# Optimization experiments

Hardware: AMD Instinct MI355X
Metric: run time of the kernel (lower is better)

Reference implementation:

```python
import jax, jax.numpy as jnp
import numpy as np

# ---- static config (matches init_kwargs) ----
OC, IC, K, S, PAD = 128, 64, 3, 1, 1
M, T, R = 5, 8, 2.5            # ALSH m, table_size, LSH bucket width r
SPAN = K * K * IC              # kernel_span = 576


def setup_inputs() -> dict:
    key = jax.random.key(0)
    k1, k2, k3, k4 = jax.random.split(key, 4)
    # xavier_uniform on the (OC, SPAN) kernel matrix
    bound = float(np.sqrt(6.0 / (OC + SPAN)))
    kernels = jax.random.uniform(k1, (OC, SPAN), minval=-bound, maxval=bound, dtype=jnp.float32)
    a = jax.random.normal(k2, (SPAN + M,), dtype=jnp.float32)          # LSH projection
    b = jax.random.uniform(k3, (), minval=0.0, maxval=R, dtype=jnp.float32)  # LSH offset
    x = jax.random.normal(k4, (16, IC, 56, 56), dtype=jnp.float32)
    return {"x": x, "kernels": kernels, "a": a, "b": b, "mode": 0}


def _im2col(x):
    # [B, SPAN, H2, W2] with feature order (C, kh, kw)
    p = jax.lax.conv_general_dilated_patches(x, (K, K), (S, S), [(PAD, PAD), (PAD, PAD)])
    B, _, H2, W2 = p.shape
    # patch matrix [SPAN, B*H2*W2]
    return p.transpose(1, 0, 2, 3).reshape(SPAN, -1), B, H2, W2


def _bucket(h):
    # floor((h+b)/r); fmod table_size; abs  (matches torch .fmod_ then .abs_)
    return jnp.abs(jnp.fmod(h.astype(jnp.int32), T))


def reference(x, kernels, a, b, mode):
    patch_matr, B, H2, W2 = _im2col(x)            # [SPAN, N], N = B*H2*W2

    # ---- vote: hash every patch column with Q-augmentation (append m halves) ----
    v = a[:SPAN] @ patch_matr + 0.5 * jnp.sum(a[SPAN:])      # [N]
    votes = _bucket(jnp.floor((v + b) / R))
    counts = jnp.zeros((T,), jnp.int32).at[votes].add(1)
    bucket = jnp.argmax(counts)                               # most common bucket

    # ---- hash table: hash each kernel row with P-augmentation (norm powers) ----
    norms2 = jnp.sum(kernels * kernels, axis=1)               # ||k||^2, [OC]
    powers = jnp.stack([norms2 ** (2 ** i) for i in range(M)], axis=1)  # ||k||^{2,4,...,2^M}
    hk = kernels @ a[:SPAN] + powers @ a[SPAN:]               # [OC]
    kidx = _bucket(jnp.floor((hk + b) / R))                   # bucket of each kernel

    # ---- select kernels in the winning bucket; scale by |rows|/OC ----
    mask = (kidx == bucket).astype(x.dtype)                   # [OC]
    cnt = jnp.sum(mask)
    # original gathers the selected rows (variable oc); we scatter back to the
    # full OC channels (zeros for inactive kernels) for static shapes.
    # empty bucket -> dense conv with all kernels, no rescale.
    factor = jnp.where(cnt > 0, mask * (OC / jnp.maximum(cnt, 1.0)), jnp.ones_like(mask))

    out = (kernels * factor[:, None]) @ patch_matr            # [OC, N]
    out = out.reshape(OC, B, H2 * W2).transpose(1, 0, 2)
    return out.reshape(B, OC, H2, W2)
```

## Files before the change

### kernel.cpp

```cpp
#include <hip/hip_runtime.h>
#include <math.h>

#define IC 64
#define OC 128
#define HH 56
#define WW 56
#define BATCH 16
#define HP 58
#define HW (HH*WW)
#define NPIX (BATCH*HW)
#define SPAN 576
#define TSIZE 8
#define VBLOCKS 196

typedef unsigned short ushort_t;
typedef unsigned int uint_t;
typedef __attribute__((ext_vector_type(8))) __bf16 bf16x8;
typedef __attribute__((ext_vector_type(4))) float f32x4;

__device__ __forceinline__ ushort_t bf16_rne(float f) {
  uint_t u = __builtin_bit_cast(uint_t, f);
  u += 0x7FFFu + ((u >> 16) & 1u);
  return (ushort_t)(u >> 16);
}

__global__ void pad_kernel(const float* __restrict__ x, ushort_t* __restrict__ xpad) {
  int idx = blockIdx.x * 256 + threadIdx.x;
  if (idx >= BATCH * HP * HP) return;
  int b = idx / (HP * HP);
  int rem = idx % (HP * HP);
  int y = rem / HP, xw = rem % HP;
  int h = y - 1, w = xw - 1;
  bool inb = ((unsigned)h < (unsigned)HH) && ((unsigned)w < (unsigned)WW);
  const float* src = x + (size_t)b * IC * HW + (inb ? h * WW + w : 0);
  uint_t* dst = (uint_t*)(xpad + (size_t)idx * IC);
  #pragma unroll
  for (int c2 = 0; c2 < IC / 2; ++c2) {
    float f0 = inb ? src[(2 * c2) * HW] : 0.0f;
    float f1 = inb ? src[(2 * c2 + 1) * HW] : 0.0f;
    dst[c2] = (uint_t)bf16_rne(f0) | ((uint_t)bf16_rne(f1) << 16);
  }
}

__global__ __launch_bounds__(256)
void tstage_kernel(const float* __restrict__ x, const float* __restrict__ a,
                   float* __restrict__ tbuf) {
  int n = blockIdx.x * 256 + threadIdx.x;
  int b = n / HW, p = n % HW;
  const float* xb = x + (size_t)b * IC * HW + p;
  float t9[9] = {0, 0, 0, 0, 0, 0, 0, 0, 0};
  #pragma unroll
  for (int c = 0; c < IC; ++c) {
    float xv = xb[(size_t)c * HW];
    #pragma unroll
    for (int tap = 0; tap < 9; ++tap) t9[tap] += a[c * 9 + tap] * xv;
  }
  float* tb = tbuf + (size_t)b * 9 * HW + p;
  #pragma unroll
  for (int tap = 0; tap < 9; ++tap) tb[(size_t)tap * HW] = t9[tap];
}

__global__ void vote2_kernel(const float* __restrict__ tbuf, const float* __restrict__ a,
                             const float* __restrict__ bptr, int* __restrict__ hist_partial) {
  __shared__ int hist[TSIZE];
  const int t = threadIdx.x;
  if (t < TSIZE) hist[t] = 0;
  __syncthreads();
  int n = blockIdx.x * 256 + t;
  int b = n / HW, p = n % HW;
  int h = p / WW, w = p % WW;
  const float* tb = tbuf + ((size_t)b * 9) * HW;
  float v = 0.0f;
  #pragma unroll
  for (int kh = 0; kh < 3; ++kh) {
    int yy = h + kh - 1;
    if ((unsigned)yy < (unsigned)HH) {
      #pragma unroll
      for (int kw = 0; kw < 3; ++kw) {
        int xx = w + kw - 1;
        if ((unsigned)xx < (unsigned)WW) v += tb[(size_t)(kh * 3 + kw) * HW + yy * WW + xx];
      }
    }
  }
  float tail = 0.5f * (a[576] + a[577] + a[578] + a[579] + a[580]);
  int hi = (int)floorf((v + tail + bptr[0]) / 2.5f);
  int r = hi % TSIZE;
  if (r < 0) r = -r;
  atomicAdd(&hist[r], 1);
  __syncthreads();
  if (t < TSIZE) hist_partial[blockIdx.x * TSIZE + t] = hist[t];
}

__global__ void w2row_kernel(const float* __restrict__ kernels, const float* __restrict__ a,
                             const float* __restrict__ bptr, ushort_t* __restrict__ w2,
                             int* __restrict__ rbucket) {
  const int r = blockIdx.x, t = threadIdx.x;
  const float* row = kernels + (size_t)r * SPAN;
  float d = 0.0f, n2 = 0.0f;
  #pragma unroll
  for (int k0 = 0; k0 < 3; ++k0) {
    int k = k0 * 256 + t;
    if (k < SPAN) { float kv = row[k]; d += kv * a[k]; n2 += kv * kv; }
  }
  __shared__ float red0[256], red1[256];
  red0[t] = d; red1[t] = n2;
  __syncthreads();
  for (int s = 128; s > 0; s >>= 1) {
    if (t < s) { red0[t] += red0[t + s]; red1[t] += red1[t + s]; }
    __syncthreads();
  }
  if (t == 0) {
    float hk = red0[0], p = red1[0];
    #pragma unroll
    for (int i = 0; i < 5; ++i) { hk += p * a[SPAN + i]; p = p * p; }
    int hi = (int)floorf((hk + bptr[0]) / 2.5f);
    int rr = hi % TSIZE;
    if (rr < 0) rr = -rr;
    rbucket[r] = rr;
  }
  #pragma unroll
  for (int j0 = 0; j0 < 3; ++j0) {
    int j = j0 * 256 + t;
    if (j < SPAN) {
      int tap = j >> 6, c = j & 63;
      w2[(size_t)r * SPAN + j] = bf16_rne(row[c * 9 + tap]);
    }
  }
}

__global__ __launch_bounds__(256, 4)
void gemm_kernel(const ushort_t* __restrict__ w2, const ushort_t* __restrict__ xpad,
                 const int* __restrict__ hist_partial, const int* __restrict__ rbucket,
                 float* __restrict__ out) {
  __shared__ ushort_t As[128 * 64];
  __shared__ ushort_t Bs[64 * 64];
  __shared__ float factor_s[OC];
  __shared__ int counts_s[TSIZE];
  __shared__ int cnt_w[4];
  const int tid = threadIdx.x;
  const int wave = tid >> 6, lane = tid & 63;
  const int n0 = blockIdx.x * 64;
  const int wm = wave * 32;

  const int srow = lane >> 3;
  const int sch = (lane & 7) ^ srow;

  int agbase[4], bgbase[2];
  #pragma unroll
  for (int i = 0; i < 4; ++i) {
    int row = wm + i * 8 + srow;
    agbase[i] = row * SPAN + sch * 8;
  }
  #pragma unroll
  for (int i = 0; i < 2; ++i) {
    int brow = wave * 16 + i * 8 + srow;
    int n = n0 + brow;
    int b = n / HW;
    int rem = n % HW;
    int h = rem / WW, w = rem % WW;
    bgbase[i] = ((b * HP + h) * HP + w) * IC + sch * 8;
  }

  f32x4 acc[2][4] = {};

  for (int tap = 0; tap < 9; ++tap) {
    const int kh = tap / 3, kw = tap % 3;
    const int toffA = tap * 64;
    const int toffB = (kh * HP + kw) * IC;
    __syncthreads();
    #pragma unroll
    for (int i = 0; i < 4; ++i)
      __builtin_amdgcn_global_load_lds(
          (const __attribute__((address_space(1))) void*)(w2 + agbase[i] + toffA),
          (__attribute__((address_space(3))) void*)(As + (wm + i * 8) * 64), 16, 0, 0);
    #pragma unroll
    for (int i = 0; i < 2; ++i)
      __builtin_amdgcn_global_load_lds(
          (const __attribute__((address_space(1))) void*)(xpad + bgbase[i] + toffB),
          (__attribute__((address_space(3))) void*)(Bs + (wave * 16 + i * 8) * 64), 16, 0, 0);
    __syncthreads();
    #pragma unroll
    for (int kk = 0; kk < 2; ++kk) {
      const int jf = kk * 4 + (lane >> 4);
      bf16x8 af[2], bfr[4];
      #pragma unroll
      for (int m = 0; m < 2; ++m) {
        int row = wm + m * 16 + (lane & 15);
        int slot = row * 8 + (jf ^ (row & 7));
        af[m] = *(const bf16x8*)(As + slot * 8);
      }
      #pragma unroll
      for (int n = 0; n < 4; ++n) {
        int col = n * 16 + (lane & 15);
        int slot = col * 8 + (jf ^ (col & 7));
        bfr[n] = *(const bf16x8*)(Bs + slot * 8);
      }
      #pragma unroll
      for (int m = 0; m < 2; ++m)
        #pragma unroll
        for (int n = 0; n < 4; ++n)
          acc[m][n] = __builtin_amdgcn_mfma_f32_16x16x32_bf16(af[m], bfr[n], acc[m][n], 0, 0, 0);
    }
  }

  if (tid < TSIZE) counts_s[tid] = 0;
  __syncthreads();
  {
    int bin = tid >> 5;
    int s = 0;
    for (int k = (tid & 31); k < VBLOCKS; k += 32) s += hist_partial[k * TSIZE + bin];
    atomicAdd(&counts_s[bin], s);
  }
  __syncthreads();
  int best = counts_s[0], bi = 0;
  #pragma unroll
  for (int i = 1; i < TSIZE; ++i) { int c = counts_s[i]; if (c > best) { best = c; bi = i; } }
  int isin = (tid < OC) ? ((rbucket[tid] == bi) ? 1 : 0) : 0;
  unsigned long long bal = __ballot(isin != 0);
  if (lane == 0) cnt_w[wave] = __popcll(bal);
  __syncthreads();
  int cnt = cnt_w[0] + cnt_w[1] + cnt_w[2] + cnt_w[3];
  if (tid < OC)
    factor_s[tid] = (cnt > 0) ? (isin ? 128.0f / (float)cnt : 0.0f) : 1.0f;
  __syncthreads();

  #pragma unroll
  for (int n = 0; n < 4; ++n) {
    int np = n0 + n * 16 + (lane & 15);
    int b = np / HW;
    int rem = np % HW;
    float* obase = out + ((size_t)b * OC) * HW + rem;
    #pragma unroll
    for (int m = 0; m < 2; ++m) {
      int ocb = wm + m * 16 + (lane >> 4) * 4;
      #pragma unroll
      for (int r = 0; r < 4; ++r) {
        obase[(size_t)(ocb + r) * HW] = acc[m][n][r] * factor_s[ocb + r];
      }
    }
  }
}

extern "C" void kernel_launch(void* const* d_in, const int* in_sizes, int n_in,
                              void* d_out, int out_size, void* d_ws, size_t ws_size,
                              hipStream_t stream) {
  (void)in_sizes; (void)n_in; (void)out_size; (void)ws_size;
  const float* x = (const float*)d_in[0];
  const float* kernels = (const float*)d_in[1];
  const float* a = (const float*)d_in[2];
  const float* b = (const float*)d_in[3];
  float* out = (float*)d_out;

  char* ws = (char*)d_ws;
  int* rbucket = (int*)ws;
  int* hist_partial = (int*)(ws + 512);
  ushort_t* w2 = (ushort_t*)(ws + 8192);
  float* tbuf = (float*)(ws + 8192 + 147456);
  ushort_t* xpad = (ushort_t*)(ws + 8192 + 147456 + 1806336);

  pad_kernel<<<211, 256, 0, stream>>>(x, xpad);
  tstage_kernel<<<VBLOCKS, 256, 0, stream>>>(x, a, tbuf);
  vote2_kernel<<<VBLOCKS, 256, 0, stream>>>(tbuf, a, b, hist_partial);
  w2row_kernel<<<OC, 256, 0, stream>>>(kernels, a, b, w2, rbucket);
  gemm_kernel<<<NPIX / 64, 256, 0, stream>>>(w2, xpad, hist_partial, rbucket, out);
}
```

Baseline: 121.9 us.

## Fuse pad, vote and weight-prep kernels into one block-dispatched prep kernel

Merges the padding, tap-projection, vote-histogram and weight-row kernels into a single launch. Blocks pick their role by block index. The vote path now keeps the per-tap projections of a two-row band plus halo rows in shared memory instead of writing and re-reading a global tbuf. This removes three launches and a global round trip. In exchange, each band recomputes the projections of its halo rows, roughly doubling that arithmetic, and the number of histogram partials the GEMM epilogue must sum grows to 448.

```diff
diff --git a/kernel.cpp b/kernel.cpp
--- a/kernel.cpp
+++ b/kernel.cpp
@@ -11,7 +11,10 @@
 #define NPIX (BATCH*HW)
 #define SPAN 576
 #define TSIZE 8
-#define VBLOCKS 196
+#define PADBLK 211
+#define VBANDS 28
+#define VBLOCKS (BATCH*VBANDS)
+#define NBLK1 (PADBLK + VBLOCKS + OC)
 
 typedef unsigned short ushort_t;
 typedef unsigned int uint_t;
@@ -24,106 +27,107 @@
   return (ushort_t)(u >> 16);
 }
 
-__global__ void pad_kernel(const float* __restrict__ x, ushort_t* __restrict__ xpad) {
-  int idx = blockIdx.x * 256 + threadIdx.x;
-  if (idx >= BATCH * HP * HP) return;
-  int b = idx / (HP * HP);
-  int rem = idx % (HP * HP);
-  int y = rem / HP, xw = rem % HP;
-  int h = y - 1, w = xw - 1;
-  bool inb = ((unsigned)h < (unsigned)HH) && ((unsigned)w < (unsigned)WW);
-  const float* src = x + (size_t)b * IC * HW + (inb ? h * WW + w : 0);
-  uint_t* dst = (uint_t*)(xpad + (size_t)idx * IC);
-  #pragma unroll
-  for (int c2 = 0; c2 < IC / 2; ++c2) {
-    float f0 = inb ? src[(2 * c2) * HW] : 0.0f;
-    float f1 = inb ? src[(2 * c2 + 1) * HW] : 0.0f;
-    dst[c2] = (uint_t)bf16_rne(f0) | ((uint_t)bf16_rne(f1) << 16);
-  }
-}
-
 __global__ __launch_bounds__(256)
-void tstage_kernel(const float* __restrict__ x, const float* __restrict__ a,
-                   float* __restrict__ tbuf) {
-  int n = blockIdx.x * 256 + threadIdx.x;
-  int b = n / HW, p = n % HW;
-  const float* xb = x + (size_t)b * IC * HW + p;
-  float t9[9] = {0, 0, 0, 0, 0, 0, 0, 0, 0};
-  #pragma unroll
-  for (int c = 0; c < IC; ++c) {
-    float xv = xb[(size_t)c * HW];
-    #pragma unroll
-    for (int tap = 0; tap < 9; ++tap) t9[tap] += a[c * 9 + tap] * xv;
-  }
-  float* tb = tbuf + (size_t)b * 9 * HW + p;
-  #pragma unroll
-  for (int tap = 0; tap < 9; ++tap) tb[(size_t)tap * HW] = t9[tap];
-}
-
-__global__ void vote2_kernel(const float* __restrict__ tbuf, const float* __restrict__ a,
-                             const float* __restrict__ bptr, int* __restrict__ hist_partial) {
+void prep_kernel(const float* __restrict__ x, const float* __restrict__ kernels,
+                 const float* __restrict__ a, const float* __restrict__ bptr,
+                 ushort_t* __restrict__ xpad, ushort_t* __restrict__ w2,
+                 int* __restrict__ rbucket, int* __restrict__ hist_partial) {
+  __shared__ float tl[224 * 9];
   __shared__ int hist[TSIZE];
-  const int t = threadIdx.x;
-  if (t < TSIZE) hist[t] = 0;
-  __syncthreads();
-  int n = blockIdx.x * 256 + t;
-  int b = n / HW, p = n % HW;
-  int h = p / WW, w = p % WW;
-  const float* tb = tbuf + ((size_t)b * 9) * HW;
-  float v = 0.0f;
-  #pragma unroll
-  for (int kh = 0; kh < 3; ++kh) {
-    int yy = h + kh - 1;
-    if ((unsigned)yy < (unsigned)HH) {
-      #pragma unroll
-      for (int kw = 0; kw < 3; ++kw) {
-        int xx = w + kw - 1;
-        if ((unsigned)xx < (unsigned)WW) v += tb[(size_t)(kh * 3 + kw) * HW + yy * WW + xx];
-      }
-    }
-  }
-  float tail = 0.5f * (a[576] + a[577] + a[578] + a[579] + a[580]);
-  int hi = (int)floorf((v + tail + bptr[0]) / 2.5f);
-  int r = hi % TSIZE;
-  if (r < 0) r = -r;
-  atomicAdd(&hist[r], 1);
-  __syncthreads();
-  if (t < TSIZE) hist_partial[blockIdx.x * TSIZE + t] = hist[t];
-}
-
-__global__ void w2row_kernel(const float* __restrict__ kernels, const float* __restrict__ a,
-                             const float* __restrict__ bptr, ushort_t* __restrict__ w2,
-                             int* __restrict__ rbucket) {
-  const int r = blockIdx.x, t = threadIdx.x;
-  const float* row = kernels + (size_t)r * SPAN;
-  float d = 0.0f, n2 = 0.0f;
-  #pragma unroll
-  for (int k0 = 0; k0 < 3; ++k0) {
-    int k = k0 * 256 + t;
-    if (k < SPAN) { float kv = row[k]; d += kv * a[k]; n2 += kv * kv; }
-  }
   __shared__ float red0[256], red1[256];
-  red0[t] = d; red1[t] = n2;
-  __syncthreads();
-  for (int s = 128; s > 0; s >>= 1) {
-    if (t < s) { red0[t] += red0[t + s]; red1[t] += red1[t + s]; }
-    __syncthreads();
-  }
-  if (t == 0) {
-    float hk = red0[0], p = red1[0];
-    #pragma unroll
-    for (int i = 0; i < 5; ++i) { hk += p * a[SPAN + i]; p = p * p; }
-    int hi = (int)floorf((hk + bptr[0]) / 2.5f);
-    int rr = hi % TSIZE;
-    if (rr < 0) rr = -rr;
-    rbucket[r] = rr;
-  }
-  #pragma unroll
-  for (int j0 = 0; j0 < 3; ++j0) {
-    int j = j0 * 256 + t;
-    if (j < SPAN) {
-      int tap = j >> 6, c = j & 63;
-      w2[(size_t)r * SPAN + j] = bf16_rne(row[c * 9 + tap]);
+  const int bx = blockIdx.x, t = threadIdx.x;
+
+  if (bx < PADBLK) {
+    int idx = bx * 256 + t;
+    if (idx >= BATCH * HP * HP) return;
+    int b = idx / (HP * HP);
+    int rem = idx % (HP * HP);
+    int y = rem / HP, xw = rem % HP;
+    int h = y - 1, w = xw - 1;
+    bool inb = ((unsigned)h < (unsigned)HH) && ((unsigned)w < (unsigned)WW);
+    const float* src = x + (size_t)b * IC * HW + (inb ? h * WW + w : 0);
+    uint_t* dst = (uint_t*)(xpad + (size_t)idx * IC);
+    #pragma unroll
+    for (int c2 = 0; c2 < IC / 2; ++c2) {
+      float f0 = inb ? src[(2 * c2) * HW] : 0.0f;
+      float f1 = inb ? src[(2 * c2 + 1) * HW] : 0.0f;
+      dst[c2] = (uint_t)bf16_rne(f0) | ((uint_t)bf16_rne(f1) << 16);
+    }
+  } else if (bx < PADBLK + VBLOCKS) {
+    const int vb = bx - PADBLK;
+    const int b = vb / VBANDS, band = vb % VBANDS;
+    const int r0 = band * 2;
+    if (t < TSIZE) hist[t] = 0;
+    if (t < 224) {
+      int prow = r0 - 1 + t / 56;
+      int col = t % 56;
+      float t9[9] = {0, 0, 0, 0, 0, 0, 0, 0, 0};
+      if ((unsigned)prow < (unsigned)HH) {
+        const float* xb = x + (size_t)b * IC * HW + prow * WW + col;
+        #pragma unroll
+        for (int c = 0; c < IC; ++c) {
+          float xv = xb[(size_t)c * HW];
+          #pragma unroll
+          for (int tap = 0; tap < 9; ++tap) t9[tap] += a[c * 9 + tap] * xv;
+        }
+      }
+      #pragma unroll
+      for (int tap = 0; tap < 9; ++tap) tl[t * 9 + tap] = t9[tap];
+    }
+    __syncthreads();
+    if (t < 112) {
+      int lr = t / 56;
+      int col = t % 56;
+      float v = 0.0f;
+      #pragma unroll
+      for (int kh = 0; kh < 3; ++kh) {
+        int gr = r0 + lr - 1 + kh;
+        #pragma unroll
+        for (int kw = 0; kw < 3; ++kw) {
+          int cc = col - 1 + kw;
+          if ((unsigned)gr < (unsigned)HH && (unsigned)cc < (unsigned)WW)
+            v += tl[((lr + kh) * 56 + cc) * 9 + (kh * 3 + kw)];
+        }
+      }
+      float tail = 0.5f * (a[576] + a[577] + a[578] + a[579] + a[580]);
+      int hi = (int)floorf((v + tail + bptr[0]) / 2.5f);
+      int r = hi % TSIZE;
+      if (r < 0) r = -r;
+      atomicAdd(&hist[r], 1);
+    }
+    __syncthreads();
+    if (t < TSIZE) hist_partial[vb * TSIZE + t] = hist[t];
+  } else {
+    const int r = bx - (PADBLK + VBLOCKS);
+    const float* row = kernels + (size_t)r * SPAN;
+    float d = 0.0f, n2 = 0.0f;
+    #pragma unroll
+    for (int k0 = 0; k0 < 3; ++k0) {
+      int k = k0 * 256 + t;
+      if (k < SPAN) { float kv = row[k]; d += kv * a[k]; n2 += kv * kv; }
+    }
+    red0[t] = d; red1[t] = n2;
+    __syncthreads();
+    for (int s = 128; s > 0; s >>= 1) {
+      if (t < s) { red0[t] += red0[t + s]; red1[t] += red1[t + s]; }
+      __syncthreads();
+    }
+    if (t == 0) {
+      float hk = red0[0], p = red1[0];
+      #pragma unroll
+      for (int i = 0; i < 5; ++i) { hk += p * a[SPAN + i]; p = p * p; }
+      int hi = (int)floorf((hk + bptr[0]) / 2.5f);
+      int rr = hi % TSIZE;
+      if (rr < 0) rr = -rr;
+      rbucket[r] = rr;
+    }
+    #pragma unroll
+    for (int j0 = 0; j0 < 3; ++j0) {
+      int j = j0 * 256 + t;
+      if (j < SPAN) {
+        int tap = j >> 6, c = j & 63;
+        w2[(size_t)r * SPAN + j] = bf16_rne(row[c * 9 + tap]);
+      }
     }
   }
 }
@@ -254,13 +258,9 @@
   char* ws = (char*)d_ws;
   int* rbucket = (int*)ws;
   int* hist_partial = (int*)(ws + 512);
-  ushort_t* w2 = (ushort_t*)(ws + 8192);
-  float* tbuf = (float*)(ws + 8192 + 147456);
-  ushort_t* xpad = (ushort_t*)(ws + 8192 + 147456 + 1806336);
-
-  pad_kernel<<<211, 256, 0, stream>>>(x, xpad);
-  tstage_kernel<<<VBLOCKS, 256, 0, stream>>>(x, a, tbuf);
-  vote2_kernel<<<VBLOCKS, 256, 0, stream>>>(tbuf, a, b, hist_partial);
-  w2row_kernel<<<OC, 256, 0, stream>>>(kernels, a, b, w2, rbucket);
+  ushort_t* w2 = (ushort_t*)(ws + 16384);
+  ushort_t* xpad = (ushort_t*)(ws + 16384 + 147456);
+
+  prep_kernel<<<NBLK1, 256, 0, stream>>>(x, kernels, a, b, xpad, w2, rbucket, hist_partial);
   gemm_kernel<<<NPIX / 64, 256, 0, stream>>>(w2, xpad, hist_partial, rbucket, out);
 }
```

Measured after the change: 109.2 us. 10.5% less time.
